# Optimization experiments

Hardware: AMD Instinct MI355X
Metric: run time of the kernel (lower is better)

Reference implementation:

```python
import jax, jax.numpy as jnp
import numpy as np

B, Q, KV, D, H = 2, 2048, 2048, 1024, 16
HD = D // H  # head dim = 64


def setup_inputs() -> dict:
    key = jax.random.key(0)
    ks = jax.random.split(key, 16)
    s = 1.0 / np.sqrt(D)
    return {
        "q": jax.random.normal(ks[0], (B, Q, D), jnp.float32),
        "k": jax.random.normal(ks[1], (B, KV, D), jnp.float32),
        "v": jax.random.normal(ks[2], (B, KV, D), jnp.float32),
        "past_k": jax.random.normal(ks[3], (B, KV, D), jnp.float32),
        "past_v": jax.random.normal(ks[4], (B, KV, D), jnp.float32),
        "mask": jax.random.randint(ks[5], (B, Q, KV + KV), 0, 2).astype(bool),
        "Wq": jax.random.uniform(ks[6], (D, D), jnp.float32, -s, s),
        "bq": jax.random.uniform(ks[7], (D,), jnp.float32, -s, s),
        "Wk": jax.random.uniform(ks[8], (D, D), jnp.float32, -s, s),
        "bk": jax.random.uniform(ks[9], (D,), jnp.float32, -s, s),
        "Wv": jax.random.uniform(ks[10], (D, D), jnp.float32, -s, s),
        "bv": jax.random.uniform(ks[11], (D,), jnp.float32, -s, s),
        "Wl": jax.random.uniform(ks[12], (D, D), jnp.float32, -s, s),
        "bl": jax.random.uniform(ks[13], (D,), jnp.float32, -s, s),
    }


def _split_heads(x):
    # (B, S, D) -> (B, H, S, HD)
    b, s, _ = x.shape
    return x.reshape(b, s, H, HD).transpose(0, 2, 1, 3)


def reference(q, k, v, past_k, past_v, mask, Wq, bq, Wk, bk, Wv, bv, Wl, bl):
    qp = q @ Wq.T + bq
    kp = k @ Wk.T + bk
    vp = v @ Wv.T + bv
    k_cat = jnp.concatenate([past_k, kp], axis=-2)  # (B, P+KV, D)
    v_cat = jnp.concatenate([past_v, vp], axis=-2)
    qh = _split_heads(qp)        # (B, H, Q, HD)
    kh = _split_heads(k_cat)     # (B, H, P+KV, HD)
    vh = _split_heads(v_cat)
    scores = jnp.einsum("bhqd,bhkd->bhqk", qh, kh) / np.sqrt(HD)
    scores = scores + mask[:, None].astype(scores.dtype) * (-10000.0)
    attn = jax.nn.softmax(scores, axis=-1)
    out = jnp.einsum("bhqk,bhkd->bhqd", attn, vh)  # (B, H, Q, HD)
    out = out.transpose(0, 2, 1, 3).reshape(q.shape[0], q.shape[1], D)
    x = out @ Wl.T + bl
    return (x, k_cat, v_cat)
```

## Files before the change

### kernel.cpp

```cpp
#include <hip/hip_runtime.h>

#define QLEN 2048
#define KVTOT 4096
#define DMODEL 1024
#define MASKC2 -14427.0f
#define SENT2  -28854.0f

typedef __attribute__((ext_vector_type(8))) short bf16x8;
typedef __attribute__((ext_vector_type(4))) float f32x4;
typedef unsigned short u16;
typedef unsigned int u32;
typedef unsigned long long u64;

__device__ __forceinline__ u16 f2b(float f) {
  union { float f; unsigned u; } v; v.f = f;
  unsigned r = v.u + 0x7FFFu + ((v.u >> 16) & 1u);
  return (u16)(r >> 16);
}

__device__ __forceinline__ float b2f(u16 x) {
  union { u32 u; float f; } v; v.u = (u32)x << 16; return v.f;
}

__device__ __forceinline__ u32 cvt_pk_bf16(float lo, float hi) {
  u32 r;
  asm("v_cvt_pk_bf16_f32 %0, %1, %2" : "=v"(r) : "v"(lo), "v"(hi));
  return r;
}

__device__ __forceinline__ float exp2v(float x) {
  float r;
  asm("v_exp_f32 %0, %1" : "=v"(r) : "v"(x));
  return r;
}

__device__ __forceinline__ float max3f(float a, float b, float c) {
  float r;
  asm("v_max3_f32 %0, %1, %2, %3" : "=v"(r) : "v"(a), "v"(b), "v"(c));
  return r;
}

__device__ __forceinline__ void gll16(const u16* g, u16* l) {
  __builtin_amdgcn_global_load_lds(
      (const __attribute__((address_space(1))) u32*)g,
      (__attribute__((address_space(3))) u32*)l, 16, 0, 0);
}

__global__ __launch_bounds__(256) void copy_past(
    const float* __restrict__ pk, const float* __restrict__ pv,
    float* __restrict__ kcat, float* __restrict__ vcat,
    u16* __restrict__ kh) {
  int i = blockIdx.x * 256 + threadIdx.x;
  int b = i >> 19;
  int r = i & 524287;
  size_t src = (size_t)i * 4;
  size_t dst = ((size_t)b * 1048576 + r) * 4;
  float4 kk = *(const float4*)&pk[src];
  float4 vv = *(const float4*)&pv[src];
  *(float4*)&kcat[dst] = kk;
  *(float4*)&vcat[dst] = vv;
  int s = r >> 8;
  int c4 = (r & 255) * 4;
  int h = c4 >> 6, d = c4 & 63;
  uint2 w = make_uint2(cvt_pk_bf16(kk.x, kk.y), cvt_pk_bf16(kk.z, kk.w));
  *(uint2*)&kh[((size_t)(b * 16 + h) * KVTOT + s) * 64 + d] = w;
}

__global__ __launch_bounds__(256) void maskpack(
    const int* __restrict__ mask, u64* __restrict__ bits) {
  int w = blockIdx.x * 4 + (threadIdx.x >> 6);
  int lane = threadIdx.x & 63;
  int mv = mask[(size_t)w * 64 + lane];
  u64 b = __ballot(mv != 0);
  if (lane == 0) bits[w] = b;
}

__global__ __launch_bounds__(256) void w2b(
    const float* __restrict__ w0, const float* __restrict__ w1,
    const float* __restrict__ w2, const float* __restrict__ w3,
    u16* __restrict__ dst) {
  const float* src = blockIdx.y == 0 ? w0 : blockIdx.y == 1 ? w1
                   : blockIdx.y == 2 ? w2 : w3;
  size_t i = ((size_t)blockIdx.x * 256 + threadIdx.x) * 8;
  float4 a = *(const float4*)&src[i];
  float4 b = *(const float4*)&src[i + 4];
  uint4 o = {cvt_pk_bf16(a.x, a.y), cvt_pk_bf16(a.z, a.w),
             cvt_pk_bf16(b.x, b.y), cvt_pk_bf16(b.z, b.w)};
  *(uint4*)&dst[(size_t)blockIdx.y * 1048576 + i] = o;
}

__global__ __launch_bounds__(256) void gemm_qkv(
    const float* __restrict__ qA, const float* __restrict__ kA,
    const float* __restrict__ vA, const u16* __restrict__ Wb,
    const float* __restrict__ bq, const float* __restrict__ bk,
    const float* __restrict__ bv,
    u16* __restrict__ qh, float* __restrict__ kcat, u16* __restrict__ kh,
    float* __restrict__ vcat) {
  const int K = 1024, N = 1024;
  __shared__ u16 As[128][32];
  __shared__ u16 Bs[128][32];
  const int z = blockIdx.z;
  const float* A = (z == 0) ? qA : (z == 1) ? kA : vA;
  const u16* W = Wb + (size_t)z * 1048576;
  const float* bias = (z == 0) ? bq : (z == 1) ? bk : bv;
  const int t = threadIdx.x;
  const int m0 = blockIdx.y * 128, n0 = blockIdx.x * 128;
  const int lane = t & 63, wid = t >> 6;
  const int wr = (wid >> 1) * 64, wc = (wid & 1) * 64;
  const int lr = lane & 15, lg = lane >> 4;
  const int ko = lg * 8;

  f32x4 acc[4][4];
  #pragma unroll
  for (int m = 0; m < 4; ++m)
    #pragma unroll
    for (int n = 0; n < 4; ++n)
      acc[m][n] = (f32x4){0.f, 0.f, 0.f, 0.f};

  for (int k0 = 0; k0 < K; k0 += 32) {
    float4 a0[2], a1[2];
    #pragma unroll
    for (int j = 0; j < 2; ++j) {
      int idx = t + j * 256;
      int r = idx >> 2, c8 = (idx & 3) * 8;
      const float* ap = A + (size_t)(m0 + r) * K + k0 + c8;
      a0[j] = *(const float4*)ap;
      a1[j] = *(const float4*)(ap + 4);
    }
    __syncthreads();
    #pragma unroll
    for (int j = 0; j < 2; ++j) {
      int idx = t + j * 256;
      int r = idx >> 2, c8 = (idx & 3) * 8;
      gll16(W + (size_t)(n0 + r) * K + k0 + c8,
            &Bs[0][0] + (size_t)(j * 256 + (t & ~63)) * 8);
      uint4 o = {cvt_pk_bf16(a0[j].x, a0[j].y), cvt_pk_bf16(a0[j].z, a0[j].w),
                 cvt_pk_bf16(a1[j].x, a1[j].y), cvt_pk_bf16(a1[j].z, a1[j].w)};
      *(uint4*)&As[r][c8] = o;
    }
    __syncthreads();
    bf16x8 av[4], bv4[4];
    #pragma unroll
    for (int m = 0; m < 4; ++m)
      av[m] = *(const bf16x8*)&As[wr + m * 16 + lr][ko];
    #pragma unroll
    for (int n = 0; n < 4; ++n)
      bv4[n] = *(const bf16x8*)&Bs[wc + n * 16 + lr][ko];
    #pragma unroll
    for (int m = 0; m < 4; ++m)
      #pragma unroll
      for (int n = 0; n < 4; ++n)
        acc[m][n] = __builtin_amdgcn_mfma_f32_16x16x32_bf16(av[m], bv4[n], acc[m][n], 0, 0, 0);
  }

  const int rq = lg * 4;
  #pragma unroll
  for (int m = 0; m < 4; ++m) {
    #pragma unroll
    for (int r = 0; r < 4; ++r) {
      int row = m0 + wr + m * 16 + rq + r;
      int bb = row >> 11, s = row & 2047;
      #pragma unroll
      for (int n = 0; n < 4; ++n) {
        int col = n0 + wc + n * 16 + lr;
        float val = acc[m][n][r] + bias[col];
        int hh = col >> 6, d = col & 63;
        if (z == 0) {
          qh[((size_t)(bb * 16 + hh) * QLEN + s) * 64 + d] = f2b(val * 0.18033688f);
        } else if (z == 1) {
          kcat[(size_t)(bb * 4096 + 2048 + s) * 1024 + col] = val;
          kh[((size_t)(bb * 16 + hh) * KVTOT + 2048 + s) * 64 + d] = f2b(val);
        } else {
          vcat[(size_t)(bb * 4096 + 2048 + s) * 1024 + col] = val;
        }
      }
    }
  }
}

__global__ __launch_bounds__(256) void gemm_out(
    const u16* __restrict__ A, const u16* __restrict__ W,
    const float* __restrict__ bias, float* __restrict__ C) {
  const int K = 1024, N = 1024;
  __shared__ u16 As[128][32];
  __shared__ u16 Bs[128][32];
  const int t = threadIdx.x;
  const int m0 = blockIdx.y * 128, n0 = blockIdx.x * 128;
  const int lane = t & 63, wid = t >> 6;
  const int wr = (wid >> 1) * 64, wc = (wid & 1) * 64;
  const int lr = lane & 15, lg = lane >> 4;
  const int ko = lg * 8;

  f32x4 acc[4][4];
  #pragma unroll
  for (int m = 0; m < 4; ++m)
    #pragma unroll
    for (int n = 0; n < 4; ++n)
      acc[m][n] = (f32x4){0.f, 0.f, 0.f, 0.f};

  for (int k0 = 0; k0 < K; k0 += 32) {
    __syncthreads();
    #pragma unroll
    for (int j = 0; j < 2; ++j) {
      int idx = t + j * 256;
      int r = idx >> 2, c8 = (idx & 3) * 8;
      size_t ldsoff = (size_t)(j * 256 + (t & ~63)) * 8;
      gll16(A + (size_t)(m0 + r) * K + k0 + c8, &As[0][0] + ldsoff);
      gll16(W + (size_t)(n0 + r) * K + k0 + c8, &Bs[0][0] + ldsoff);
    }
    __syncthreads();
    bf16x8 av[4], bv4[4];
    #pragma unroll
    for (int m = 0; m < 4; ++m)
      av[m] = *(const bf16x8*)&As[wr + m * 16 + lr][ko];
    #pragma unroll
    for (int n = 0; n < 4; ++n)
      bv4[n] = *(const bf16x8*)&Bs[wc + n * 16 + lr][ko];
    #pragma unroll
    for (int m = 0; m < 4; ++m)
      #pragma unroll
      for (int n = 0; n < 4; ++n)
        acc[m][n] = __builtin_amdgcn_mfma_f32_16x16x32_bf16(av[m], bv4[n], acc[m][n], 0, 0, 0);
  }

  const int rq = lg * 4;
  #pragma unroll
  for (int m = 0; m < 4; ++m) {
    #pragma unroll
    for (int r = 0; r < 4; ++r) {
      int row = m0 + wr + m * 16 + rq + r;
      float* cp = C + (size_t)row * N;
      #pragma unroll
      for (int n = 0; n < 4; ++n) {
        int col = n0 + wc + n * 16 + lr;
        cp[col] = acc[m][n][r] + bias[col];
      }
    }
  }
}

__global__ __launch_bounds__(256) void repack_vt(
    const float* __restrict__ src, u16* __restrict__ dst) {
  __shared__ u16 T[64][72];
  const int t = threadIdx.x;
  const int kv0 = blockIdx.x * 64;
  const int bh = blockIdx.y;
  const int b = bh >> 4, h = bh & 15;
  #pragma unroll
  for (int it = 0; it < 4; ++it) {
    int idx = t + it * 256;
    int r = idx >> 4;
    int c4 = (idx & 15) * 4;
    float4 v = *(const float4*)(src + (size_t)(b * KVTOT + kv0 + r) * DMODEL + h * 64 + c4);
    *(uint2*)&T[r][c4] = make_uint2(cvt_pk_bf16(v.x, v.y), cvt_pk_bf16(v.z, v.w));
  }
  __syncthreads();
  #pragma unroll
  for (int it = 0; it < 2; ++it) {
    int idx = t + it * 256;
    int d = idx & 63;
    int kc8 = (idx >> 6) * 8;
    bf16x8 o;
    #pragma unroll
    for (int j = 0; j < 8; ++j) o[j] = (short)T[kc8 + j][d];
    *(bf16x8*)(dst + (size_t)((b * 16 + h) * 64 + d) * KVTOT + kv0 + kc8) = o;
  }
}

__global__ __launch_bounds__(256, 2) void attn_mfma(
    const u16* __restrict__ qh, const u16* __restrict__ kh,
    const u16* __restrict__ vt, const u64* __restrict__ mbits,
    u16* __restrict__ out) {
  __shared__ __align__(16) u16 shm[4 * 64 * 72];
  __shared__ float mM[4][64];
  __shared__ float mL[4][64];
  const int t = threadIdx.x;
  const int wid = t >> 6, lane = t & 63;
  const int lr = lane & 15, lg = lane >> 4;
  const int fid = blockIdx.x;
  const int virt = (fid & 7) * 128 + (fid >> 3);
  const int bh = virt >> 5, qt = virt & 31;
  const int b = bh >> 4, h = bh & 15;
  const int q0 = qt * 64;

  u16* bufA = shm + wid * 2304;
  u16* bufB = bufA + 1152;

  bf16x8 ones;
  #pragma unroll
  for (int j = 0; j < 8; ++j) ones[j] = (short)0x3F80;

  bf16x8 qf[4][2];
  #pragma unroll
  for (int i = 0; i < 4; ++i) {
    const u16* qp = qh + ((size_t)bh * QLEN + q0 + i * 16 + lr) * 64 + lg * 8;
    qf[i][0] = *(const bf16x8*)qp;
    qf[i][1] = *(const bf16x8*)(qp + 32);
  }

  const u16* kbase = kh + (size_t)bh * KVTOT * 64 + (size_t)wid * 1024 * 64;
  const u16* vbase = vt + (size_t)bh * 64 * KVTOT + wid * 1024;
  const u64* mbase = mbits + ((size_t)b * QLEN + q0 + lr) * 64 + wid * 16;

  float mprev[4] = {SENT2, SENT2, SENT2, SENT2};
  f32x4 oacc[4][4];
  f32x4 oaccL[4];
  #pragma unroll
  for (int i = 0; i < 4; ++i) {
    oaccL[i] = (f32x4){0.f, 0.f, 0.f, 0.f};
    #pragma unroll
    for (int dt = 0; dt < 4; ++dt) oacc[i][dt] = (f32x4){0.f, 0.f, 0.f, 0.f};
  }

  bf16x8 kf[4][2];
  #pragma unroll
  for (int tile = 0; tile < 4; ++tile) {
    const u16* kp = kbase + (size_t)(tile * 16 + lr) * 64 + lg * 8;
    kf[tile][0] = *(const bf16x8*)kp;
    kf[tile][1] = *(const bf16x8*)(kp + 32);
  }

  bf16x8 vf[4][2];

  auto QK = [&](int i, f32x4* sacc, u64 mb) {
    u64 mq = mb >> (lg * 4);
    const float negm = -mprev[i], negmm = MASKC2 - mprev[i];
    #pragma unroll
    for (int tile = 0; tile < 4; ++tile) {
      unsigned nib = (unsigned)((mq >> (tile * 16)) & 0xFull);
      #pragma unroll
      for (int r = 0; r < 4; ++r)
        sacc[tile][r] = (nib & (1u << r)) ? negmm : negm;
    }
    __builtin_amdgcn_s_setprio(1);
    #pragma unroll
    for (int tile = 0; tile < 4; ++tile) {
      sacc[tile] = __builtin_amdgcn_mfma_f32_16x16x32_bf16(kf[tile][0], qf[i][0], sacc[tile], 0, 0, 0);
      sacc[tile] = __builtin_amdgcn_mfma_f32_16x16x32_bf16(kf[tile][1], qf[i][1], sacc[tile], 0, 0, 0);
    }
    __builtin_amdgcn_s_setprio(0);
  };

  auto SM = [&](int i, f32x4* sacc, u16* pbuf) {
    float t1 = max3f(sacc[0][0], sacc[0][1], sacc[0][2]);
    float t2 = max3f(sacc[0][3], sacc[1][0], sacc[1][1]);
    float t3 = max3f(sacc[1][2], sacc[1][3], sacc[2][0]);
    float t4 = max3f(sacc[2][1], sacc[2][2], sacc[2][3]);
    float t5 = max3f(sacc[3][0], sacc[3][1], sacc[3][2]);
    float lmax = fmaxf(sacc[3][3], t1);
    lmax = max3f(lmax, t2, t3);
    lmax = max3f(lmax, t4, t5);
    if (!__all(lmax <= 11.0f)) {
      float rmax = fmaxf(lmax, __shfl_xor(lmax, 16));
      rmax = fmaxf(rmax, __shfl_xor(rmax, 32));
      float shift = fmaxf(rmax, 0.f);
      float corr = exp2v(-shift);
      float cr[4];
      #pragma unroll
      for (int r = 0; r < 4; ++r) cr[r] = __shfl(corr, lg * 4 + r);
      #pragma unroll
      for (int dt = 0; dt < 4; ++dt)
        #pragma unroll
        for (int r = 0; r < 4; ++r) oacc[i][dt][r] *= cr[r];
      #pragma unroll
      for (int r = 0; r < 4; ++r) oaccL[i][r] *= cr[r];
      mprev[i] += shift;
      #pragma unroll
      for (int tile = 0; tile < 4; ++tile)
        #pragma unroll
        for (int r = 0; r < 4; ++r) sacc[tile][r] -= shift;
    }
    #pragma unroll
    for (int tile = 0; tile < 4; ++tile) {
      float p0 = exp2v(sacc[tile][0]);
      float p1 = exp2v(sacc[tile][1]);
      float p2 = exp2v(sacc[tile][2]);
      float p3 = exp2v(sacc[tile][3]);
      *(uint2*)&pbuf[lr * 72 + tile * 16 + lg * 4] =
          make_uint2(cvt_pk_bf16(p0, p1), cvt_pk_bf16(p2, p3));
    }
  };

  auto PV = [&](int i, const u16* pbuf) {
    bf16x8 pa0 = *(const bf16x8*)&pbuf[lr * 72 + lg * 8];
    bf16x8 pa1 = *(const bf16x8*)&pbuf[lr * 72 + 32 + lg * 8];
    __builtin_amdgcn_s_setprio(1);
    #pragma unroll
    for (int dt = 0; dt < 4; ++dt) {
      oacc[i][dt] = __builtin_amdgcn_mfma_f32_16x16x32_bf16(pa0, vf[dt][0], oacc[i][dt], 0, 0, 0);
      oacc[i][dt] = __builtin_amdgcn_mfma_f32_16x16x32_bf16(pa1, vf[dt][1], oacc[i][dt], 0, 0, 0);
    }
    oaccL[i] = __builtin_amdgcn_mfma_f32_16x16x32_bf16(pa0, ones, oaccL[i], 0, 0, 0);
    oaccL[i] = __builtin_amdgcn_mfma_f32_16x16x32_bf16(pa1, ones, oaccL[i], 0, 0, 0);
    __builtin_amdgcn_s_setprio(0);
  };

  f32x4 sA[4], sB[4];

  for (int it = 0; it < 16; ++it) {
    u64 mbv[4];
    #pragma unroll
    for (int i = 0; i < 4; ++i) mbv[i] = mbase[(size_t)i * 1024 + it];

    const u16* vp = vbase + it * 64;
    #pragma unroll
    for (int dt = 0; dt < 4; ++dt) {
      const u16* vq = vp + (size_t)(dt * 16 + lr) * KVTOT + lg * 8;
      vf[dt][0] = *(const bf16x8*)vq;
      vf[dt][1] = *(const bf16x8*)(vq + 32);
    }

    QK(0, sA, mbv[0]);
    SM(0, sA, bufA);
    QK(1, sB, mbv[1]);
    PV(0, bufA);
    SM(1, sB, bufB);
    QK(2, sA, mbv[2]);
    PV(1, bufB);
    SM(2, sA, bufA);
    QK(3, sB, mbv[3]);
    PV(2, bufA);
    SM(3, sB, bufB);
    if (it + 1 < 16) {
      const u16* kp = kbase + (size_t)(it + 1) * 4096;
      #pragma unroll
      for (int tile = 0; tile < 4; ++tile) {
        const u16* kq = kp + (size_t)(tile * 16 + lr) * 64 + lg * 8;
        kf[tile][0] = *(const bf16x8*)kq;
        kf[tile][1] = *(const bf16x8*)(kq + 32);
      }
    }
    PV(3, bufB);
  }

  __syncthreads();
  u16* mo = shm + wid * 4608;
  #pragma unroll
  for (int i = 0; i < 4; ++i)
    #pragma unroll
    for (int dt = 0; dt < 4; ++dt)
      #pragma unroll
      for (int r = 0; r < 4; ++r)
        mo[(i * 16 + lg * 4 + r) * 72 + dt * 16 + lr] = f2b(oacc[i][dt][r]);
  if (lr == 0) {
    #pragma unroll
    for (int i = 0; i < 4; ++i)
      #pragma unroll
      for (int r = 0; r < 4; ++r)
        mL[wid][i * 16 + lg * 4 + r] = oaccL[i][r];
  }
  if (lg == 0) {
    #pragma unroll
    for (int i = 0; i < 4; ++i) mM[wid][i * 16 + lr] = mprev[i];
  }
  __syncthreads();

  const int q = wid * 16 + lr;
  float m0 = mM[0][q], m1 = mM[1][q], m2 = mM[2][q], m3 = mM[3][q];
  float mm = fmaxf(max3f(m0, m1, m2), m3);
  float w0 = exp2v(m0 - mm), w1 = exp2v(m1 - mm);
  float w2 = exp2v(m2 - mm), w3 = exp2v(m3 - mm);
  float l = mL[0][q] * w0 + mL[1][q] * w1 + mL[2][q] * w2 + mL[3][q] * w3;
  float inv = 1.f / l;
  float wgt[4] = {w0 * inv, w1 * inv, w2 * inv, w3 * inv};
  float o[16];
  #pragma unroll
  for (int j = 0; j < 16; ++j) o[j] = 0.f;
  #pragma unroll
  for (int w = 0; w < 4; ++w) {
    const u16* src = shm + w * 4608 + q * 72 + lg * 16;
    bf16x8 a0 = *(const bf16x8*)src;
    bf16x8 a1 = *(const bf16x8*)(src + 8);
    #pragma unroll
    for (int j = 0; j < 8; ++j) {
      o[j]     += b2f((u16)a0[j]) * wgt[w];
      o[8 + j] += b2f((u16)a1[j]) * wgt[w];
    }
  }
  u16* op = out + ((size_t)b * QLEN + q0 + q) * DMODEL + h * 64 + lg * 16;
  uint4 wA = {cvt_pk_bf16(o[0], o[1]), cvt_pk_bf16(o[2], o[3]),
              cvt_pk_bf16(o[4], o[5]), cvt_pk_bf16(o[6], o[7])};
  uint4 wB = {cvt_pk_bf16(o[8], o[9]), cvt_pk_bf16(o[10], o[11]),
              cvt_pk_bf16(o[12], o[13]), cvt_pk_bf16(o[14], o[15])};
  *(uint4*)op = wA;
  *(uint4*)(op + 8) = wB;
}

extern "C" void kernel_launch(void* const* d_in, const int* in_sizes, int n_in,
                              void* d_out, int out_size, void* d_ws, size_t ws_size,
                              hipStream_t stream) {
  const float* q      = (const float*)d_in[0];
  const float* k      = (const float*)d_in[1];
  const float* v      = (const float*)d_in[2];
  const float* past_k = (const float*)d_in[3];
  const float* past_v = (const float*)d_in[4];
  const int*   mask   = (const int*)d_in[5];
  const float* Wq     = (const float*)d_in[6];
  const float* bq     = (const float*)d_in[7];
  const float* Wk     = (const float*)d_in[8];
  const float* bk     = (const float*)d_in[9];
  const float* Wv     = (const float*)d_in[10];
  const float* bv     = (const float*)d_in[11];
  const float* Wl     = (const float*)d_in[12];
  const float* bl     = (const float*)d_in[13];

  float* xout = (float*)d_out;
  float* kcat = xout + 4194304;
  float* vcat = xout + 12582912;

  u16* wsb = (u16*)d_ws;
  u16* attno = wsb;
  u16* qh = wsb + 4194304;
  u16* kh = wsb + 8388608;
  u16* vt = wsb + 16777216;
  u16* Wb = wsb + 25165824;
  u64* mbits = (u64*)(wsb + 29360128);

  copy_past<<<4096, 256, 0, stream>>>(past_k, past_v, kcat, vcat, kh);
  maskpack<<<65536, 256, 0, stream>>>(mask, mbits);
  w2b<<<dim3(512, 4), 256, 0, stream>>>(Wq, Wk, Wv, Wl, Wb);

  gemm_qkv<<<dim3(8, 32, 3), 256, 0, stream>>>(
      q, k, v, Wb, bq, bk, bv, qh, kcat, kh, vcat);

  repack_vt<<<dim3(64, 32), 256, 0, stream>>>(vcat, vt);

  attn_mfma<<<1024, 256, 0, stream>>>(qh, kh, vt, mbits, attno);

  gemm_out<<<dim3(8, 32), 256, 0, stream>>>(attno, Wb + 3145728, bl, xout);
}
```

Before: 312.1 us.

## Halve attention query tile to 32 rows, doubling grid and occupancy

The attention kernel now handles 32 query rows per block instead of 64. The grid doubles to 2048 blocks and launch bounds rise to 3 blocks per CU, and the merge epilogue is remapped so each lane writes 8 output columns. The aim is lower register and LDS use, giving more waves per CU and better latency hiding. In exchange, every K/V tile is loaded twice as often per query, so more global and L2 traffic goes to K, V and the mask bits. The QK/softmax/PV software pipeline also gets shorter, leaving less overlap inside each iteration.

Measured after the change: 419.4 us. 1.34x slower.

```diff
diff --git a/kernel.cpp b/kernel.cpp
--- a/kernel.cpp
+++ b/kernel.cpp
@@ -267,21 +267,21 @@
   }
 }
 
-__global__ __launch_bounds__(256, 2) void attn_mfma(
+__global__ __launch_bounds__(256, 3) void attn_mfma(
     const u16* __restrict__ qh, const u16* __restrict__ kh,
     const u16* __restrict__ vt, const u64* __restrict__ mbits,
     u16* __restrict__ out) {
-  __shared__ __align__(16) u16 shm[4 * 64 * 72];
-  __shared__ float mM[4][64];
-  __shared__ float mL[4][64];
+  __shared__ __align__(16) u16 shm[4 * 32 * 72];
+  __shared__ float mM[4][32];
+  __shared__ float mL[4][32];
   const int t = threadIdx.x;
   const int wid = t >> 6, lane = t & 63;
   const int lr = lane & 15, lg = lane >> 4;
   const int fid = blockIdx.x;
-  const int virt = (fid & 7) * 128 + (fid >> 3);
-  const int bh = virt >> 5, qt = virt & 31;
+  const int virt = (fid & 7) * 256 + (fid >> 3);
+  const int bh = virt >> 6, qt = virt & 63;
   const int b = bh >> 4, h = bh & 15;
-  const int q0 = qt * 64;
+  const int q0 = qt * 32;
 
   u16* bufA = shm + wid * 2304;
   u16* bufB = bufA + 1152;
@@ -290,9 +290,9 @@
   #pragma unroll
   for (int j = 0; j < 8; ++j) ones[j] = (short)0x3F80;
 
-  bf16x8 qf[4][2];
-  #pragma unroll
-  for (int i = 0; i < 4; ++i) {
+  bf16x8 qf[2][2];
+  #pragma unroll
+  for (int i = 0; i < 2; ++i) {
     const u16* qp = qh + ((size_t)bh * QLEN + q0 + i * 16 + lr) * 64 + lg * 8;
     qf[i][0] = *(const bf16x8*)qp;
     qf[i][1] = *(const bf16x8*)(qp + 32);
@@ -302,11 +302,11 @@
   const u16* vbase = vt + (size_t)bh * 64 * KVTOT + wid * 1024;
   const u64* mbase = mbits + ((size_t)b * QLEN + q0 + lr) * 64 + wid * 16;
 
-  float mprev[4] = {SENT2, SENT2, SENT2, SENT2};
-  f32x4 oacc[4][4];
-  f32x4 oaccL[4];
-  #pragma unroll
-  for (int i = 0; i < 4; ++i) {
+  float mprev[2] = {SENT2, SENT2};
+  f32x4 oacc[2][4];
+  f32x4 oaccL[2];
+  #pragma unroll
+  for (int i = 0; i < 2; ++i) {
     oaccL[i] = (f32x4){0.f, 0.f, 0.f, 0.f};
     #pragma unroll
     for (int dt = 0; dt < 4; ++dt) oacc[i][dt] = (f32x4){0.f, 0.f, 0.f, 0.f};
@@ -398,9 +398,8 @@
   f32x4 sA[4], sB[4];
 
   for (int it = 0; it < 16; ++it) {
-    u64 mbv[4];
-    #pragma unroll
-    for (int i = 0; i < 4; ++i) mbv[i] = mbase[(size_t)i * 1024 + it];
+    u64 mbv0 = mbase[it];
+    u64 mbv1 = mbase[1024 + it];
 
     const u16* vp = vbase + it * 64;
     #pragma unroll
@@ -410,17 +409,11 @@
       vf[dt][1] = *(const bf16x8*)(vq + 32);
     }
 
-    QK(0, sA, mbv[0]);
+    QK(0, sA, mbv0);
     SM(0, sA, bufA);
-    QK(1, sB, mbv[1]);
+    QK(1, sB, mbv1);
     PV(0, bufA);
     SM(1, sB, bufB);
-    QK(2, sA, mbv[2]);
-    PV(1, bufB);
-    SM(2, sA, bufA);
-    QK(3, sB, mbv[3]);
-    PV(2, bufA);
-    SM(3, sB, bufB);
     if (it + 1 < 16) {
       const u16* kp = kbase + (size_t)(it + 1) * 4096;
       #pragma unroll
@@ -430,13 +423,13 @@
         kf[tile][1] = *(const bf16x8*)(kq + 32);
       }
     }
-    PV(3, bufB);
+    PV(1, bufB);
   }
 
   __syncthreads();
-  u16* mo = shm + wid * 4608;
-  #pragma unroll
-  for (int i = 0; i < 4; ++i)
+  u16* mo = shm + wid * 2304;
+  #pragma unroll
+  for (int i = 0; i < 2; ++i)
     #pragma unroll
     for (int dt = 0; dt < 4; ++dt)
       #pragma unroll
@@ -444,46 +437,39 @@
         mo[(i * 16 + lg * 4 + r) * 72 + dt * 16 + lr] = f2b(oacc[i][dt][r]);
   if (lr == 0) {
     #pragma unroll
-    for (int i = 0; i < 4; ++i)
+    for (int i = 0; i < 2; ++i)
       #pragma unroll
       for (int r = 0; r < 4; ++r)
         mL[wid][i * 16 + lg * 4 + r] = oaccL[i][r];
   }
   if (lg == 0) {
     #pragma unroll
-    for (int i = 0; i < 4; ++i) mM[wid][i * 16 + lr] = mprev[i];
+    for (int i = 0; i < 2; ++i) mM[wid][i * 16 + lr] = mprev[i];
   }
   __syncthreads();
 
-  const int q = wid * 16 + lr;
-  float m0 = mM[0][q], m1 = mM[1][q], m2 = mM[2][q], m3 = mM[3][q];
+  const int ql = wid * 8 + (lane >> 3);
+  const int dc = (lane & 7) * 8;
+  float m0 = mM[0][ql], m1 = mM[1][ql], m2 = mM[2][ql], m3 = mM[3][ql];
   float mm = fmaxf(max3f(m0, m1, m2), m3);
   float w0 = exp2v(m0 - mm), w1 = exp2v(m1 - mm);
   float w2 = exp2v(m2 - mm), w3 = exp2v(m3 - mm);
-  float l = mL[0][q] * w0 + mL[1][q] * w1 + mL[2][q] * w2 + mL[3][q] * w3;
+  float l = mL[0][ql] * w0 + mL[1][ql] * w1 + mL[2][ql] * w2 + mL[3][ql] * w3;
   float inv = 1.f / l;
   float wgt[4] = {w0 * inv, w1 * inv, w2 * inv, w3 * inv};
-  float o[16];
-  #pragma unroll
-  for (int j = 0; j < 16; ++j) o[j] = 0.f;
+  float o[8];
+  #pragma unroll
+  for (int j = 0; j < 8; ++j) o[j] = 0.f;
   #pragma unroll
   for (int w = 0; w < 4; ++w) {
-    const u16* src = shm + w * 4608 + q * 72 + lg * 16;
-    bf16x8 a0 = *(const bf16x8*)src;
-    bf16x8 a1 = *(const bf16x8*)(src + 8);
-    #pragma unroll
-    for (int j = 0; j < 8; ++j) {
-      o[j]     += b2f((u16)a0[j]) * wgt[w];
-      o[8 + j] += b2f((u16)a1[j]) * wgt[w];
-    }
-  }
-  u16* op = out + ((size_t)b * QLEN + q0 + q) * DMODEL + h * 64 + lg * 16;
+    bf16x8 a0 = *(const bf16x8*)(shm + w * 2304 + ql * 72 + dc);
+    #pragma unroll
+    for (int j = 0; j < 8; ++j) o[j] += b2f((u16)a0[j]) * wgt[w];
+  }
+  u16* op = out + ((size_t)b * QLEN + q0 + ql) * DMODEL + h * 64 + dc;
   uint4 wA = {cvt_pk_bf16(o[0], o[1]), cvt_pk_bf16(o[2], o[3]),
               cvt_pk_bf16(o[4], o[5]), cvt_pk_bf16(o[6], o[7])};
-  uint4 wB = {cvt_pk_bf16(o[8], o[9]), cvt_pk_bf16(o[10], o[11]),
-              cvt_pk_bf16(o[12], o[13]), cvt_pk_bf16(o[14], o[15])};
   *(uint4*)op = wA;
-  *(uint4*)(op + 8) = wB;
 }
 
 extern "C" void kernel_launch(void* const* d_in, const int* in_sizes, int n_in,
@@ -525,7 +511,7 @@
 
   repack_vt<<<dim3(64, 32), 256, 0, stream>>>(vcat, vt);
 
-  attn_mfma<<<1024, 256, 0, stream>>>(qh, kh, vt, mbits, attno);
+  attn_mfma<<<2048, 256, 0, stream>>>(qh, kh, vt, mbits, attno);
 
   gemm_out<<<dim3(8, 32), 256, 0, stream>>>(attno, Wb + 3145728, bl, xout);
 }
```

## Pre-convert QKV activations to bf16 and load them into LDS asynchronously

Applied to the files above, without the earlier changes.

Adds a separate kernel that converts the q, k, v fp32 activations to bf16 into scratch buffers (reusing the attno and vt workspace regions). The QKV GEMM then loads both A and W tiles with direct global-to-LDS loads instead of loading fp32 into registers and converting in-loop. This cuts in-loop register pressure and A-tile traffic, at the cost of an extra pass over the activations. Separately, the attention loop moves the next K-tile prefetch earlier, ahead of the PV(2)/SM(3) steps, to hide more load latency.

Result: faster. 301.4 us (-3.4%).

```diff
diff --git a/kernel.cpp b/kernel.cpp
--- a/kernel.cpp
+++ b/kernel.cpp
@@ -89,9 +89,24 @@
   *(uint4*)&dst[(size_t)blockIdx.y * 1048576 + i] = o;
 }
 
+__global__ __launch_bounds__(256) void a2b(
+    const float* __restrict__ a0, const float* __restrict__ a1,
+    const float* __restrict__ a2, u16* __restrict__ dst0,
+    u16* __restrict__ dst12) {
+  const int y = blockIdx.y;
+  const float* src = y == 0 ? a0 : y == 1 ? a1 : a2;
+  u16* dst = y == 0 ? dst0 : dst12 + (size_t)(y - 1) * 4194304;
+  size_t i = ((size_t)blockIdx.x * 256 + threadIdx.x) * 8;
+  float4 a = *(const float4*)&src[i];
+  float4 b = *(const float4*)&src[i + 4];
+  uint4 o = {cvt_pk_bf16(a.x, a.y), cvt_pk_bf16(a.z, a.w),
+             cvt_pk_bf16(b.x, b.y), cvt_pk_bf16(b.z, b.w)};
+  *(uint4*)&dst[i] = o;
+}
+
 __global__ __launch_bounds__(256) void gemm_qkv(
-    const float* __restrict__ qA, const float* __restrict__ kA,
-    const float* __restrict__ vA, const u16* __restrict__ Wb,
+    const u16* __restrict__ Ab0, const u16* __restrict__ Ab12,
+    const u16* __restrict__ Wb,
     const float* __restrict__ bq, const float* __restrict__ bk,
     const float* __restrict__ bv,
     u16* __restrict__ qh, float* __restrict__ kcat, u16* __restrict__ kh,
@@ -100,7 +115,7 @@
   __shared__ u16 As[128][32];
   __shared__ u16 Bs[128][32];
   const int z = blockIdx.z;
-  const float* A = (z == 0) ? qA : (z == 1) ? kA : vA;
+  const u16* A = (z == 0) ? Ab0 : Ab12 + (size_t)(z - 1) * 4194304;
   const u16* W = Wb + (size_t)z * 1048576;
   const float* bias = (z == 0) ? bq : (z == 1) ? bk : bv;
   const int t = threadIdx.x;
@@ -118,25 +133,14 @@
       acc[m][n] = (f32x4){0.f, 0.f, 0.f, 0.f};
 
   for (int k0 = 0; k0 < K; k0 += 32) {
-    float4 a0[2], a1[2];
+    __syncthreads();
     #pragma unroll
     for (int j = 0; j < 2; ++j) {
       int idx = t + j * 256;
       int r = idx >> 2, c8 = (idx & 3) * 8;
-      const float* ap = A + (size_t)(m0 + r) * K + k0 + c8;
-      a0[j] = *(const float4*)ap;
-      a1[j] = *(const float4*)(ap + 4);
-    }
-    __syncthreads();
-    #pragma unroll
-    for (int j = 0; j < 2; ++j) {
-      int idx = t + j * 256;
-      int r = idx >> 2, c8 = (idx & 3) * 8;
-      gll16(W + (size_t)(n0 + r) * K + k0 + c8,
-            &Bs[0][0] + (size_t)(j * 256 + (t & ~63)) * 8);
-      uint4 o = {cvt_pk_bf16(a0[j].x, a0[j].y), cvt_pk_bf16(a0[j].z, a0[j].w),
-                 cvt_pk_bf16(a1[j].x, a1[j].y), cvt_pk_bf16(a1[j].z, a1[j].w)};
-      *(uint4*)&As[r][c8] = o;
+      size_t ldsoff = (size_t)(j * 256 + (t & ~63)) * 8;
+      gll16(A + (size_t)(m0 + r) * K + k0 + c8, &As[0][0] + ldsoff);
+      gll16(W + (size_t)(n0 + r) * K + k0 + c8, &Bs[0][0] + ldsoff);
     }
     __syncthreads();
     bf16x8 av[4], bv4[4];
@@ -419,8 +423,6 @@
     PV(1, bufB);
     SM(2, sA, bufA);
     QK(3, sB, mbv[3]);
-    PV(2, bufA);
-    SM(3, sB, bufB);
     if (it + 1 < 16) {
       const u16* kp = kbase + (size_t)(it + 1) * 4096;
       #pragma unroll
@@ -430,6 +432,8 @@
         kf[tile][1] = *(const bf16x8*)(kq + 32);
       }
     }
+    PV(2, bufA);
+    SM(3, sB, bufB);
     PV(3, bufB);
   }
 
@@ -519,9 +523,10 @@
   copy_past<<<4096, 256, 0, stream>>>(past_k, past_v, kcat, vcat, kh);
   maskpack<<<65536, 256, 0, stream>>>(mask, mbits);
   w2b<<<dim3(512, 4), 256, 0, stream>>>(Wq, Wk, Wv, Wl, Wb);
+  a2b<<<dim3(2048, 3), 256, 0, stream>>>(q, k, v, attno, vt);
 
   gemm_qkv<<<dim3(8, 32, 3), 256, 0, stream>>>(
-      q, k, v, Wb, bq, bk, bv, qh, kcat, kh, vcat);
+      attno, vt, Wb, bq, bk, bv, qh, kcat, kh, vcat);
 
   repack_vt<<<dim3(64, 32), 256, 0, stream>>>(vcat, vt);
 
```
